# Performance work log

Measured on AMD Instinct MI355X. Metric: run time of the kernel, lower is better.

Reference implementation:

```python
import jax, jax.numpy as jnp
import numpy as np

T, D, I, E, K = 2048, 2048, 5632, 8, 2


def setup_inputs() -> dict:
    key = jax.random.key(0)
    k1, k2, k3, k4, k5 = jax.random.split(key, 5)
    s = 0.02
    return {
        "x": jax.random.normal(k1, (T, D), dtype=jnp.float32),
        "gate_w": jax.random.normal(k2, (E, D), dtype=jnp.float32) * s,
        "w_gate": jax.random.normal(k3, (E, I, D), dtype=jnp.float32) * s,
        "w_up": jax.random.normal(k4, (E, I, D), dtype=jnp.float32) * s,
        "w_down": jax.random.normal(k5, (E, D, I), dtype=jnp.float32) * s,
    }


def reference(x, gate_w, w_gate, w_up, w_down):
    # Router: logits [T, E], top-k then softmax over the k selected logits
    logits = x @ gate_w.T
    top_vals, top_idx = jax.lax.top_k(logits, K)          # [T, K]
    rw = jax.nn.softmax(top_vals, axis=-1)                # [T, K]
    # Dense combine weights [T, E]: sum of routing weights over selected slots.
    # Mathematically identical to the per-(expert, slot) scatter-add in torch,
    # since duplicate selections of the same expert just sum their weights.
    combine = jnp.sum(jax.nn.one_hot(top_idx, E, dtype=x.dtype) * rw[..., None], axis=1)  # [T, E]
    # SwiGLU expert MLPs, batched over experts (grouped GEMM as dense einsum)
    g = jnp.einsum("td,eid->tei", x, w_gate)              # [T, E, I]
    u = jnp.einsum("td,eid->tei", x, w_up)                # [T, E, I]
    h = jax.nn.silu(g) * u                                 # [T, E, I]
    out_e = jnp.einsum("tei,edi->ted", h, w_down)         # [T, E, D]
    return jnp.einsum("ted,te->td", out_e, combine)       # [T, D]
```

## Files before the change

kernel.cpp:

```cpp
#include <hip/hip_runtime.h>
#include <hip/hip_bf16.h>
#include <stdint.h>

#define TTOK 2048
#define DDIM 2048
#define IDIM 5632
#define NEXP 8

typedef __attribute__((ext_vector_type(8))) short bf16x8;
typedef __attribute__((ext_vector_type(4))) float f32x4;
typedef __attribute__((ext_vector_type(8))) unsigned short u16x8;
typedef __attribute__((ext_vector_type(4))) unsigned short u16x4;

__device__ __forceinline__ unsigned short f2bf(float f) {
  union { float f; uint32_t u; } v; v.f = f;
  uint32_t u = v.u + 0x7fffu + ((v.u >> 16) & 1u);
  return (unsigned short)(u >> 16);
}

__device__ __forceinline__ uint32_t fbits(float f) {
  union { float f; uint32_t u; } v; v.f = f; return v.u;
}

__device__ __forceinline__ u16x8 cvt8t(float4 a, float4 b) {
  union { u16x8 v; uint32_t w[4]; } r;
  r.w[0] = __builtin_amdgcn_perm(fbits(a.y), fbits(a.x), 0x07060302);
  r.w[1] = __builtin_amdgcn_perm(fbits(a.w), fbits(a.z), 0x07060302);
  r.w[2] = __builtin_amdgcn_perm(fbits(b.y), fbits(b.x), 0x07060302);
  r.w[3] = __builtin_amdgcn_perm(fbits(b.w), fbits(b.z), 0x07060302);
  return r.v;
}

typedef __attribute__((address_space(3))) void lds_t;
typedef const __attribute__((address_space(1))) void gbl_t;
__device__ __forceinline__ void gload16(const void* g, void* l) {
  __builtin_amdgcn_global_load_lds((gbl_t*)g, (lds_t*)l, 16, 0, 0);
}

#define PIPE_WAIT_BAR() asm volatile("s_waitcnt vmcnt(8) lgkmcnt(0)\n\ts_barrier" ::: "memory")

__global__ __launch_bounds__(256) void router_kernel(
    const float* __restrict__ x, const float* __restrict__ gw,
    unsigned short* __restrict__ xbf,
    int* __restrict__ cnt, int* __restrict__ slots, float* __restrict__ wts)
{
  const int lane = threadIdx.x & 63;
  const int t = (blockIdx.x * blockDim.x + threadIdx.x) >> 6;
  const float* xr = x + (size_t)t * DDIM;
  float acc[NEXP];
#pragma unroll
  for (int e = 0; e < NEXP; ++e) acc[e] = 0.f;
#pragma unroll
  for (int it = 0; it < DDIM / 256; ++it) {
    const int d = (it * 64 + lane) * 4;
    const float4 xv = *(const float4*)(xr + d);
    u16x4 xb; xb[0]=f2bf(xv.x); xb[1]=f2bf(xv.y); xb[2]=f2bf(xv.z); xb[3]=f2bf(xv.w);
    *(u16x4*)(xbf + (size_t)t * DDIM + d) = xb;
#pragma unroll
    for (int e = 0; e < NEXP; ++e) {
      const float4 gv = *(const float4*)(gw + (size_t)e * DDIM + d);
      acc[e] += xv.x*gv.x + xv.y*gv.y + xv.z*gv.z + xv.w*gv.w;
    }
  }
#pragma unroll
  for (int e = 0; e < NEXP; ++e) {
    float v = acc[e];
#pragma unroll
    for (int off = 32; off > 0; off >>= 1) v += __shfl_xor(v, off);
    acc[e] = v;
  }
  if (lane == 0) {
    int i0 = 0; float v0 = acc[0];
#pragma unroll
    for (int e = 1; e < NEXP; ++e) if (acc[e] > v0) { v0 = acc[e]; i0 = e; }
    int i1 = -1; float v1 = -3.4e38f;
#pragma unroll
    for (int e = 0; e < NEXP; ++e) { if (e == i0) continue; if (acc[e] > v1) { v1 = acc[e]; i1 = e; } }
    const float e1 = __expf(v1 - v0);
    const float w0 = 1.f / (1.f + e1);
    const float w1 = e1 / (1.f + e1);
    const int p0 = atomicAdd(&cnt[i0], 1);
    slots[i0 * TTOK + p0] = t * 2;     wts[i0 * TTOK + p0] = w0;
    const int p1 = atomicAdd(&cnt[i1], 1);
    slots[i1 * TTOK + p1] = t * 2 + 1; wts[i1 * TTOK + p1] = w1;
  }
}

__global__ void plan_kernel(const int* __restrict__ cnt,
                            int* __restrict__ tilemap, int* __restrict__ ntiles)
{
  if (threadIdx.x == 0 && blockIdx.x == 0) {
    int n = 0;
#pragma unroll
    for (int e = 0; e < NEXP; ++e) {
      const int nt = (cnt[e] + 127) >> 7;
      for (int m = 0; m < nt; ++m) tilemap[n++] = (e << 8) | m;
    }
    ntiles[0] = n;
  }
}


__global__ __launch_bounds__(256) void gateup_kernel(
    const unsigned short* __restrict__ xbf,
    const float* __restrict__ wg, const float* __restrict__ wu,
    const int* __restrict__ cnt, const int* __restrict__ slots,
    const int* __restrict__ tilemap, const int* __restrict__ ntiles,
    unsigned short* __restrict__ h)
{
  const int flat = (blockIdx.x & 7) * 440 + (blockIdx.x >> 3);
  const int ti = flat % 40;
  if (ti >= ntiles[0]) return;
  const int em = tilemap[ti];
  const int e = em >> 8;
  const int mt = em & 255;
  const int n0 = (flat / 40) * 64;
  const int count = cnt[e];
  const int m0 = mt * 128;

  __shared__ unsigned short A[2][128][64];
  __shared__ unsigned short Bg[2][64][64];
  __shared__ unsigned short Bu[2][64][64];
  __shared__ int rslot[128];
  __shared__ int rtok[128];

  const int tid = threadIdx.x;
  const int lane = tid & 63;
  const int wid = tid >> 6;

  if (tid < 128) {
    const int idx = m0 + tid;
    const int safe = slots[e * TTOK + m0];
    const int s = (idx < count) ? slots[e * TTOK + idx] : safe;
    rslot[tid] = (idx < count) ? s : -1;
    rtok[tid] = s >> 1;
  }
  __syncthreads();

  const int aswz = ((lane & 7) ^ ((lane >> 3) & 7)) * 8;
  const unsigned short* aptr[4];
#pragma unroll
  for (int j = 0; j < 4; ++j) {
    const int arow = wid * 32 + j * 8 + (lane >> 3);
    aptr[j] = xbf + (size_t)rtok[arow] * DDIM + aswz;
  }

  const int brow = tid >> 2;
  const int bcb = (tid & 3) * 2;
  const int bswz = brow & 7;
  const size_t wboff = (size_t)e * IDIM * DDIM + (size_t)(n0 + brow) * DDIM + bcb * 8;
  const float* gsrc = wg + wboff;
  const float* usrc = wu + wboff;

  const int wr = wid >> 1, wc = wid & 1;
  const int fr = lane & 15;
  const int kc = lane >> 4;
  const int rsw = fr & 7;

  f32x4 accg[4][2] = {};
  f32x4 accu[4][2] = {};

  float4 Pg[4], Pu[4];
#pragma unroll
  for (int j = 0; j < 4; ++j) gload16(aptr[j], &A[0][wid * 32][0] + j * 512);
#pragma unroll
  for (int q = 0; q < 4; ++q) { Pg[q] = *(const float4*)(gsrc + q * 4); Pu[q] = *(const float4*)(usrc + q * 4); }
#pragma unroll
  for (int qq = 0; qq < 2; ++qq) {
    const int oc = ((bcb + qq) ^ bswz) * 8;
    *(u16x8*)&Bg[0][brow][oc] = cvt8t(Pg[qq * 2], Pg[qq * 2 + 1]);
    *(u16x8*)&Bu[0][brow][oc] = cvt8t(Pu[qq * 2], Pu[qq * 2 + 1]);
  }
#pragma unroll
  for (int q = 0; q < 4; ++q) { Pg[q] = *(const float4*)(gsrc + 64 + q * 4); Pu[q] = *(const float4*)(usrc + 64 + q * 4); }
  PIPE_WAIT_BAR();

#pragma unroll 2
  for (int t = 0; t < 32; ++t) {
    const int cur = t & 1;
    const int kp  = (t + 1 <= 31) ? (t + 1) * 64 : 31 * 64;
    const int kp2 = (t + 2 <= 31) ? (t + 2) * 64 : 31 * 64;

#pragma unroll
    for (int j = 0; j < 4; ++j) gload16(aptr[j] + kp, &A[cur ^ 1][wid * 32][0] + j * 512);
    __builtin_amdgcn_sched_barrier(0);
#pragma unroll
    for (int qq = 0; qq < 2; ++qq) {
      const int oc = ((bcb + qq) ^ bswz) * 8;
      *(u16x8*)&Bg[cur ^ 1][brow][oc] = cvt8t(Pg[qq * 2], Pg[qq * 2 + 1]);
      *(u16x8*)&Bu[cur ^ 1][brow][oc] = cvt8t(Pu[qq * 2], Pu[qq * 2 + 1]);
    }
#pragma unroll
    for (int q = 0; q < 4; ++q) { Pg[q] = *(const float4*)(gsrc + kp2 + q * 4); Pu[q] = *(const float4*)(usrc + kp2 + q * 4); }
    __builtin_amdgcn_sched_barrier(0);

    __builtin_amdgcn_s_setprio(1);
#pragma unroll
    for (int kk = 0; kk < 2; ++kk) {
      bf16x8 a[4], bg[2], bu[2];
      const int cs = ((kk * 4 + kc) ^ rsw) * 8;
#pragma unroll
      for (int mf = 0; mf < 4; ++mf)
        a[mf] = *(const bf16x8*)&A[cur][wr * 64 + mf * 16 + fr][cs];
#pragma unroll
      for (int nf = 0; nf < 2; ++nf) {
        bg[nf] = *(const bf16x8*)&Bg[cur][wc * 32 + nf * 16 + fr][cs];
        bu[nf] = *(const bf16x8*)&Bu[cur][wc * 32 + nf * 16 + fr][cs];
      }
#pragma unroll
      for (int mf = 0; mf < 4; ++mf)
#pragma unroll
        for (int nf = 0; nf < 2; ++nf) {
          accg[mf][nf] = __builtin_amdgcn_mfma_f32_16x16x32_bf16(a[mf], bg[nf], accg[mf][nf], 0, 0, 0);
          accu[mf][nf] = __builtin_amdgcn_mfma_f32_16x16x32_bf16(a[mf], bu[nf], accu[mf][nf], 0, 0, 0);
        }
    }
    __builtin_amdgcn_s_setprio(0);

    PIPE_WAIT_BAR();
  }

#pragma unroll
  for (int mf = 0; mf < 4; ++mf)
#pragma unroll
    for (int nf = 0; nf < 2; ++nf)
#pragma unroll
      for (int j = 0; j < 4; ++j) {
        const int r = wr * 64 + mf * 16 + (lane >> 4) * 4 + j;
        const int s = rslot[r];
        if (s >= 0) {
          const float g = accg[mf][nf][j];
          const float u = accu[mf][nf][j];
          const float hv = g / (1.f + __expf(-g)) * u;
          h[(size_t)s * IDIM + n0 + wc * 32 + nf * 16 + fr] = f2bf(hv);
        }
      }
}

__global__ __launch_bounds__(256) void down_kernel(
    const unsigned short* __restrict__ h,
    const float* __restrict__ wd,
    const int* __restrict__ cnt, const int* __restrict__ slots,
    const float* __restrict__ wts,
    const int* __restrict__ tilemap, const int* __restrict__ ntiles,
    float* __restrict__ out)
{
  const int flat = (blockIdx.x & 7) * 160 + (blockIdx.x >> 3);
  const int ti = flat % 40;
  if (ti >= ntiles[0]) return;
  const int em = tilemap[ti];
  const int e = em >> 8;
  const int mt = em & 255;
  const int r2 = flat / 40;
  const int n0 = (r2 & 15) * 128;
  const int ks = r2 >> 4;
  const int kbase = ks * (IDIM / 2);
  const int count = cnt[e];
  const int m0 = mt * 128;

  __shared__ unsigned short A[2][128][64];
  __shared__ unsigned short B[2][128][64];
  __shared__ int rslot[128];
  __shared__ float rw[128];

  const int tid = threadIdx.x;
  const int lane = tid & 63;
  const int wid = tid >> 6;

  if (tid < 128) {
    const int idx = m0 + tid;
    const int safe = slots[e * TTOK + m0];
    const int s = (idx < count) ? slots[e * TTOK + idx] : safe;
    rslot[tid] = (idx < count) ? s : (safe | 0x40000000);
    rw[tid] = (idx < count) ? wts[e * TTOK + idx] : 0.f;
  }
  __syncthreads();

  const int aswz = ((lane & 7) ^ ((lane >> 3) & 7)) * 8;
  const unsigned short* aptr[4];
#pragma unroll
  for (int j = 0; j < 4; ++j) {
    const int arow = wid * 32 + j * 8 + (lane >> 3);
    aptr[j] = h + (size_t)(rslot[arow] & 0x3fffffff) * IDIM + kbase + aswz;
  }

  const int brow = tid >> 1;
  const int bcb = (tid & 1) * 4;
  const int bswz = brow & 7;
  const float* bsrc = wd + (size_t)e * DDIM * IDIM + (size_t)(n0 + brow) * IDIM + kbase + bcb * 8;

  const int wr = wid >> 1, wc = wid & 1;
  const int fr = lane & 15;
  const int kc = lane >> 4;
  const int rsw = fr & 7;

  f32x4 acc[4][4] = {};

  float4 Pb[8];
#pragma unroll
  for (int j = 0; j < 4; ++j) gload16(aptr[j], &A[0][wid * 32][0] + j * 512);
#pragma unroll
  for (int q = 0; q < 8; ++q) Pb[q] = *(const float4*)(bsrc + q * 4);
#pragma unroll
  for (int qq = 0; qq < 4; ++qq)
    *(u16x8*)&B[0][brow][((bcb + qq) ^ bswz) * 8] = cvt8t(Pb[qq * 2], Pb[qq * 2 + 1]);
#pragma unroll
  for (int q = 0; q < 8; ++q) Pb[q] = *(const float4*)(bsrc + 64 + q * 4);
  PIPE_WAIT_BAR();

#pragma unroll 2
  for (int t = 0; t < 44; ++t) {
    const int cur = t & 1;
    const int kp  = (t + 1 <= 43) ? (t + 1) * 64 : 43 * 64;
    const int kp2 = (t + 2 <= 43) ? (t + 2) * 64 : 43 * 64;

#pragma unroll
    for (int j = 0; j < 4; ++j) gload16(aptr[j] + kp, &A[cur ^ 1][wid * 32][0] + j * 512);
    __builtin_amdgcn_sched_barrier(0);
#pragma unroll
    for (int qq = 0; qq < 4; ++qq)
      *(u16x8*)&B[cur ^ 1][brow][((bcb + qq) ^ bswz) * 8] = cvt8t(Pb[qq * 2], Pb[qq * 2 + 1]);
#pragma unroll
    for (int q = 0; q < 8; ++q) Pb[q] = *(const float4*)(bsrc + kp2 + q * 4);
    __builtin_amdgcn_sched_barrier(0);

    __builtin_amdgcn_s_setprio(1);
#pragma unroll
    for (int kk = 0; kk < 2; ++kk) {
      bf16x8 a[4], b[4];
      const int cs = ((kk * 4 + kc) ^ rsw) * 8;
#pragma unroll
      for (int mf = 0; mf < 4; ++mf)
        a[mf] = *(const bf16x8*)&A[cur][wr * 64 + mf * 16 + fr][cs];
#pragma unroll
      for (int nf = 0; nf < 4; ++nf)
        b[nf] = *(const bf16x8*)&B[cur][wc * 64 + nf * 16 + fr][cs];
#pragma unroll
      for (int mf = 0; mf < 4; ++mf)
#pragma unroll
        for (int nf = 0; nf < 4; ++nf)
          acc[mf][nf] = __builtin_amdgcn_mfma_f32_16x16x32_bf16(a[mf], b[nf], acc[mf][nf], 0, 0, 0);
    }
    __builtin_amdgcn_s_setprio(0);

    PIPE_WAIT_BAR();
  }

#pragma unroll
  for (int mf = 0; mf < 4; ++mf)
#pragma unroll
    for (int j = 0; j < 4; ++j) {
      const int r = wr * 64 + mf * 16 + (lane >> 4) * 4 + j;
      const int s = rslot[r];
      if (!(s & 0x40000000)) {
        const int t2 = s >> 1;
        const float w = rw[r];
#pragma unroll
        for (int nf = 0; nf < 4; ++nf)
          atomicAdd(out + (size_t)t2 * DDIM + n0 + wc * 64 + nf * 16 + fr,
                    acc[mf][nf][j] * w);
      }
    }
}

extern "C" void kernel_launch(void* const* d_in, const int* in_sizes, int n_in,
                              void* d_out, int out_size, void* d_ws, size_t ws_size,
                              hipStream_t stream) {
  const float* x  = (const float*)d_in[0];
  const float* gw = (const float*)d_in[1];
  const float* wg = (const float*)d_in[2];
  const float* wu = (const float*)d_in[3];
  const float* wd = (const float*)d_in[4];
  float* out = (float*)d_out;

  char* ws = (char*)d_ws;
  unsigned short* xbf = (unsigned short*)ws;
  unsigned short* h   = (unsigned short*)(ws + 8388608);
  int*   slots = (int*)(ws + 8388608 + 46137344);
  float* wts   = (float*)(ws + 8388608 + 46137344 + 65536);
  int*   cnt   = (int*)(ws + 8388608 + 46137344 + 131072);
  int*   tmap  = (int*)(ws + 8388608 + 46137344 + 131072 + 32);
  int*   ntl   = (int*)(ws + 8388608 + 46137344 + 131072 + 288);

  hipMemsetAsync(cnt, 0, NEXP * sizeof(int), stream);
  hipMemsetAsync(d_out, 0, (size_t)TTOK * DDIM * sizeof(float), stream);

  router_kernel<<<TTOK / 4, 256, 0, stream>>>(x, gw, xbf, cnt, slots, wts);
  plan_kernel<<<1, 64, 0, stream>>>(cnt, tmap, ntl);
  gateup_kernel<<<3520, 256, 0, stream>>>(xbf, wg, wu, cnt, slots, tmap, ntl, h);
  down_kernel<<<1280, 256, 0, stream>>>(h, wd, cnt, slots, wts, tmap, ntl, out);
}
```

Measured before the change: 858.2 us.

## Split gate/up GEMMs across warp groups and halve down-proj N tile

```diff
diff --git a/kernel.cpp b/kernel.cpp
--- a/kernel.cpp
+++ b/kernel.cpp
@@ -37,7 +37,7 @@
   __builtin_amdgcn_global_load_lds((gbl_t*)g, (lds_t*)l, 16, 0, 0);
 }
 
-#define PIPE_WAIT_BAR() asm volatile("s_waitcnt vmcnt(8) lgkmcnt(0)\n\ts_barrier" ::: "memory")
+#define PIPE_BAR() asm volatile("s_waitcnt vmcnt(4) lgkmcnt(0)\n\ts_barrier" ::: "memory")
 
 __global__ __launch_bounds__(256) void router_kernel(
     const float* __restrict__ x, const float* __restrict__ gw,
@@ -101,7 +101,7 @@
 }
 
 
-__global__ __launch_bounds__(256) void gateup_kernel(
+__global__ __launch_bounds__(512, 4) void gateup_kernel(
     const unsigned short* __restrict__ xbf,
     const float* __restrict__ wg, const float* __restrict__ wu,
     const int* __restrict__ cnt, const int* __restrict__ slots,
@@ -138,42 +138,41 @@
   __syncthreads();
 
   const int aswz = ((lane & 7) ^ ((lane >> 3) & 7)) * 8;
-  const unsigned short* aptr[4];
-#pragma unroll
-  for (int j = 0; j < 4; ++j) {
-    const int arow = wid * 32 + j * 8 + (lane >> 3);
+  const unsigned short* aptr[2];
+#pragma unroll
+  for (int j = 0; j < 2; ++j) {
+    const int arow = wid * 16 + j * 8 + (lane >> 3);
     aptr[j] = xbf + (size_t)rtok[arow] * DDIM + aswz;
   }
 
-  const int brow = tid >> 2;
-  const int bcb = (tid & 3) * 2;
+  const int mat = wid >> 2;
+  unsigned short (*Bm)[64][64] = (mat == 0) ? Bg : Bu;
+  const float* wsel = (mat == 0) ? wg : wu;
+
+  const int tidm = tid & 255;
+  const int brow = tidm >> 2;
+  const int bcb = (tidm & 3) * 2;
   const int bswz = brow & 7;
-  const size_t wboff = (size_t)e * IDIM * DDIM + (size_t)(n0 + brow) * DDIM + bcb * 8;
-  const float* gsrc = wg + wboff;
-  const float* usrc = wu + wboff;
-
-  const int wr = wid >> 1, wc = wid & 1;
+  const float* msrc = wsel + (size_t)e * IDIM * DDIM + (size_t)(n0 + brow) * DDIM + bcb * 8;
+
+  const int wr = (wid >> 1) & 1, wc = wid & 1;
   const int fr = lane & 15;
   const int kc = lane >> 4;
   const int rsw = fr & 7;
 
-  f32x4 accg[4][2] = {};
-  f32x4 accu[4][2] = {};
-
-  float4 Pg[4], Pu[4];
-#pragma unroll
-  for (int j = 0; j < 4; ++j) gload16(aptr[j], &A[0][wid * 32][0] + j * 512);
-#pragma unroll
-  for (int q = 0; q < 4; ++q) { Pg[q] = *(const float4*)(gsrc + q * 4); Pu[q] = *(const float4*)(usrc + q * 4); }
-#pragma unroll
-  for (int qq = 0; qq < 2; ++qq) {
-    const int oc = ((bcb + qq) ^ bswz) * 8;
-    *(u16x8*)&Bg[0][brow][oc] = cvt8t(Pg[qq * 2], Pg[qq * 2 + 1]);
-    *(u16x8*)&Bu[0][brow][oc] = cvt8t(Pu[qq * 2], Pu[qq * 2 + 1]);
-  }
-#pragma unroll
-  for (int q = 0; q < 4; ++q) { Pg[q] = *(const float4*)(gsrc + 64 + q * 4); Pu[q] = *(const float4*)(usrc + 64 + q * 4); }
-  PIPE_WAIT_BAR();
+  f32x4 acc[4][2] = {};
+
+  float4 P[4];
+#pragma unroll
+  for (int j = 0; j < 2; ++j) gload16(aptr[j], &A[0][wid * 16][0] + j * 512);
+#pragma unroll
+  for (int q = 0; q < 4; ++q) P[q] = *(const float4*)(msrc + q * 4);
+#pragma unroll
+  for (int qq = 0; qq < 2; ++qq)
+    *(u16x8*)&Bm[0][brow][((bcb + qq) ^ bswz) * 8] = cvt8t(P[qq * 2], P[qq * 2 + 1]);
+#pragma unroll
+  for (int q = 0; q < 4; ++q) P[q] = *(const float4*)(msrc + 64 + q * 4);
+  PIPE_BAR();
 
 #pragma unroll 2
   for (int t = 0; t < 32; ++t) {
@@ -182,62 +181,73 @@
     const int kp2 = (t + 2 <= 31) ? (t + 2) * 64 : 31 * 64;
 
 #pragma unroll
-    for (int j = 0; j < 4; ++j) gload16(aptr[j] + kp, &A[cur ^ 1][wid * 32][0] + j * 512);
+    for (int j = 0; j < 2; ++j) gload16(aptr[j] + kp, &A[cur ^ 1][wid * 16][0] + j * 512);
     __builtin_amdgcn_sched_barrier(0);
 #pragma unroll
-    for (int qq = 0; qq < 2; ++qq) {
-      const int oc = ((bcb + qq) ^ bswz) * 8;
-      *(u16x8*)&Bg[cur ^ 1][brow][oc] = cvt8t(Pg[qq * 2], Pg[qq * 2 + 1]);
-      *(u16x8*)&Bu[cur ^ 1][brow][oc] = cvt8t(Pu[qq * 2], Pu[qq * 2 + 1]);
-    }
-#pragma unroll
-    for (int q = 0; q < 4; ++q) { Pg[q] = *(const float4*)(gsrc + kp2 + q * 4); Pu[q] = *(const float4*)(usrc + kp2 + q * 4); }
+    for (int qq = 0; qq < 2; ++qq)
+      *(u16x8*)&Bm[cur ^ 1][brow][((bcb + qq) ^ bswz) * 8] = cvt8t(P[qq * 2], P[qq * 2 + 1]);
+#pragma unroll
+    for (int q = 0; q < 4; ++q) P[q] = *(const float4*)(msrc + kp2 + q * 4);
     __builtin_amdgcn_sched_barrier(0);
 
     __builtin_amdgcn_s_setprio(1);
 #pragma unroll
     for (int kk = 0; kk < 2; ++kk) {
-      bf16x8 a[4], bg[2], bu[2];
+      bf16x8 a[4], b[2];
       const int cs = ((kk * 4 + kc) ^ rsw) * 8;
 #pragma unroll
       for (int mf = 0; mf < 4; ++mf)
         a[mf] = *(const bf16x8*)&A[cur][wr * 64 + mf * 16 + fr][cs];
 #pragma unroll
-      for (int nf = 0; nf < 2; ++nf) {
-        bg[nf] = *(const bf16x8*)&Bg[cur][wc * 32 + nf * 16 + fr][cs];
-        bu[nf] = *(const bf16x8*)&Bu[cur][wc * 32 + nf * 16 + fr][cs];
-      }
+      for (int nf = 0; nf < 2; ++nf)
+        b[nf] = *(const bf16x8*)&Bm[cur][wc * 32 + nf * 16 + fr][cs];
 #pragma unroll
       for (int mf = 0; mf < 4; ++mf)
 #pragma unroll
-        for (int nf = 0; nf < 2; ++nf) {
-          accg[mf][nf] = __builtin_amdgcn_mfma_f32_16x16x32_bf16(a[mf], bg[nf], accg[mf][nf], 0, 0, 0);
-          accu[mf][nf] = __builtin_amdgcn_mfma_f32_16x16x32_bf16(a[mf], bu[nf], accu[mf][nf], 0, 0, 0);
-        }
+        for (int nf = 0; nf < 2; ++nf)
+          acc[mf][nf] = __builtin_amdgcn_mfma_f32_16x16x32_bf16(a[mf], b[nf], acc[mf][nf], 0, 0, 0);
     }
     __builtin_amdgcn_s_setprio(0);
 
-    PIPE_WAIT_BAR();
-  }
-
-#pragma unroll
-  for (int mf = 0; mf < 4; ++mf)
-#pragma unroll
-    for (int nf = 0; nf < 2; ++nf)
-#pragma unroll
-      for (int j = 0; j < 4; ++j) {
-        const int r = wr * 64 + mf * 16 + (lane >> 4) * 4 + j;
-        const int s = rslot[r];
-        if (s >= 0) {
-          const float g = accg[mf][nf][j];
-          const float u = accu[mf][nf][j];
-          const float hv = g / (1.f + __expf(-g)) * u;
-          h[(size_t)s * IDIM + n0 + wc * 32 + nf * 16 + fr] = f2bf(hv);
+    PIPE_BAR();
+  }
+
+  __syncthreads();
+  float* uex = (float*)&A[0][0][0];
+  if (mat == 1) {
+#pragma unroll
+    for (int mf = 0; mf < 4; ++mf)
+#pragma unroll
+      for (int nf = 0; nf < 2; ++nf)
+#pragma unroll
+        for (int j = 0; j < 4; ++j) {
+          const int r = wr * 64 + mf * 16 + (lane >> 4) * 4 + j;
+          const int c = wc * 32 + nf * 16 + fr;
+          uex[r * 64 + c] = acc[mf][nf][j];
         }
-      }
-}
-
-__global__ __launch_bounds__(256) void down_kernel(
+  }
+  __syncthreads();
+  if (mat == 0) {
+#pragma unroll
+    for (int mf = 0; mf < 4; ++mf)
+#pragma unroll
+      for (int nf = 0; nf < 2; ++nf)
+#pragma unroll
+        for (int j = 0; j < 4; ++j) {
+          const int r = wr * 64 + mf * 16 + (lane >> 4) * 4 + j;
+          const int c = wc * 32 + nf * 16 + fr;
+          const int s = rslot[r];
+          if (s >= 0) {
+            const float g = acc[mf][nf][j];
+            const float u = uex[r * 64 + c];
+            const float hv = g / (1.f + __expf(-g)) * u;
+            h[(size_t)s * IDIM + n0 + c] = f2bf(hv);
+          }
+        }
+  }
+}
+
+__global__ __launch_bounds__(256, 4) void down_kernel(
     const unsigned short* __restrict__ h,
     const float* __restrict__ wd,
     const int* __restrict__ cnt, const int* __restrict__ slots,
@@ -245,21 +255,20 @@
     const int* __restrict__ tilemap, const int* __restrict__ ntiles,
     float* __restrict__ out)
 {
-  const int flat = (blockIdx.x & 7) * 160 + (blockIdx.x >> 3);
+  const int flat = (blockIdx.x & 7) * 320 + (blockIdx.x >> 3);
   const int ti = flat % 40;
   if (ti >= ntiles[0]) return;
   const int em = tilemap[ti];
   const int e = em >> 8;
   const int mt = em & 255;
-  const int r2 = flat / 40;
-  const int n0 = (r2 & 15) * 128;
-  const int ks = r2 >> 4;
-  const int kbase = ks * (IDIM / 2);
+  const int rest = flat / 40;
+  const int n0 = (rest & 31) * 64;
+  const int kbase = (rest >> 5) * (IDIM / 2);
   const int count = cnt[e];
   const int m0 = mt * 128;
 
   __shared__ unsigned short A[2][128][64];
-  __shared__ unsigned short B[2][128][64];
+  __shared__ unsigned short B[2][64][64];
   __shared__ int rslot[128];
   __shared__ float rw[128];
 
@@ -284,8 +293,8 @@
     aptr[j] = h + (size_t)(rslot[arow] & 0x3fffffff) * IDIM + kbase + aswz;
   }
 
-  const int brow = tid >> 1;
-  const int bcb = (tid & 1) * 4;
+  const int brow = tid >> 2;
+  const int bcb = (tid & 3) * 2;
   const int bswz = brow & 7;
   const float* bsrc = wd + (size_t)e * DDIM * IDIM + (size_t)(n0 + brow) * IDIM + kbase + bcb * 8;
 
@@ -294,19 +303,19 @@
   const int kc = lane >> 4;
   const int rsw = fr & 7;
 
-  f32x4 acc[4][4] = {};
-
-  float4 Pb[8];
+  f32x4 acc[4][2] = {};
+
+  float4 P[4];
 #pragma unroll
   for (int j = 0; j < 4; ++j) gload16(aptr[j], &A[0][wid * 32][0] + j * 512);
 #pragma unroll
-  for (int q = 0; q < 8; ++q) Pb[q] = *(const float4*)(bsrc + q * 4);
-#pragma unroll
-  for (int qq = 0; qq < 4; ++qq)
-    *(u16x8*)&B[0][brow][((bcb + qq) ^ bswz) * 8] = cvt8t(Pb[qq * 2], Pb[qq * 2 + 1]);
-#pragma unroll
-  for (int q = 0; q < 8; ++q) Pb[q] = *(const float4*)(bsrc + 64 + q * 4);
-  PIPE_WAIT_BAR();
+  for (int q = 0; q < 4; ++q) P[q] = *(const float4*)(bsrc + q * 4);
+#pragma unroll
+  for (int qq = 0; qq < 2; ++qq)
+    *(u16x8*)&B[0][brow][((bcb + qq) ^ bswz) * 8] = cvt8t(P[qq * 2], P[qq * 2 + 1]);
+#pragma unroll
+  for (int q = 0; q < 4; ++q) P[q] = *(const float4*)(bsrc + 64 + q * 4);
+  asm volatile("s_waitcnt vmcnt(4) lgkmcnt(0)\n\ts_barrier" ::: "memory");
 
 #pragma unroll 2
   for (int t = 0; t < 44; ++t) {
@@ -318,32 +327,32 @@
     for (int j = 0; j < 4; ++j) gload16(aptr[j] + kp, &A[cur ^ 1][wid * 32][0] + j * 512);
     __builtin_amdgcn_sched_barrier(0);
 #pragma unroll
-    for (int qq = 0; qq < 4; ++qq)
-      *(u16x8*)&B[cur ^ 1][brow][((bcb + qq) ^ bswz) * 8] = cvt8t(Pb[qq * 2], Pb[qq * 2 + 1]);
-#pragma unroll
-    for (int q = 0; q < 8; ++q) Pb[q] = *(const float4*)(bsrc + kp2 + q * 4);
+    for (int qq = 0; qq < 2; ++qq)
+      *(u16x8*)&B[cur ^ 1][brow][((bcb + qq) ^ bswz) * 8] = cvt8t(P[qq * 2], P[qq * 2 + 1]);
+#pragma unroll
+    for (int q = 0; q < 4; ++q) P[q] = *(const float4*)(bsrc + kp2 + q * 4);
     __builtin_amdgcn_sched_barrier(0);
 
     __builtin_amdgcn_s_setprio(1);
 #pragma unroll
     for (int kk = 0; kk < 2; ++kk) {
-      bf16x8 a[4], b[4];
+      bf16x8 a[4], b[2];
       const int cs = ((kk * 4 + kc) ^ rsw) * 8;
 #pragma unroll
       for (int mf = 0; mf < 4; ++mf)
         a[mf] = *(const bf16x8*)&A[cur][wr * 64 + mf * 16 + fr][cs];
 #pragma unroll
-      for (int nf = 0; nf < 4; ++nf)
-        b[nf] = *(const bf16x8*)&B[cur][wc * 64 + nf * 16 + fr][cs];
+      for (int nf = 0; nf < 2; ++nf)
+        b[nf] = *(const bf16x8*)&B[cur][wc * 32 + nf * 16 + fr][cs];
 #pragma unroll
       for (int mf = 0; mf < 4; ++mf)
 #pragma unroll
-        for (int nf = 0; nf < 4; ++nf)
+        for (int nf = 0; nf < 2; ++nf)
           acc[mf][nf] = __builtin_amdgcn_mfma_f32_16x16x32_bf16(a[mf], b[nf], acc[mf][nf], 0, 0, 0);
     }
     __builtin_amdgcn_s_setprio(0);
 
-    PIPE_WAIT_BAR();
+    asm volatile("s_waitcnt vmcnt(4) lgkmcnt(0)\n\ts_barrier" ::: "memory");
   }
 
 #pragma unroll
@@ -356,8 +365,8 @@
         const int t2 = s >> 1;
         const float w = rw[r];
 #pragma unroll
-        for (int nf = 0; nf < 4; ++nf)
-          atomicAdd(out + (size_t)t2 * DDIM + n0 + wc * 64 + nf * 16 + fr,
+        for (int nf = 0; nf < 2; ++nf)
+          atomicAdd(out + (size_t)t2 * DDIM + n0 + wc * 32 + nf * 16 + fr,
                     acc[mf][nf][j] * w);
       }
     }
@@ -387,6 +396,6 @@
 
   router_kernel<<<TTOK / 4, 256, 0, stream>>>(x, gw, xbf, cnt, slots, wts);
   plan_kernel<<<1, 64, 0, stream>>>(cnt, tmap, ntl);
-  gateup_kernel<<<3520, 256, 0, stream>>>(xbf, wg, wu, cnt, slots, tmap, ntl, h);
-  down_kernel<<<1280, 256, 0, stream>>>(h, wd, cnt, slots, wts, tmap, ntl, out);
-}
+  gateup_kernel<<<3520, 512, 0, stream>>>(xbf, wg, wu, cnt, slots, tmap, ntl, h);
+  down_kernel<<<2560, 256, 0, stream>>>(h, wd, cnt, slots, wts, tmap, ntl, out);
+}
```

Result: faster. 806.6 us (-6.0%).
